# Performance work log

Hardware: AMD Instinct MI355X
Metric: run time of the kernel (lower is better)

The kernel has to match this reference:

```python
import jax, jax.numpy as jnp
import numpy as np

B, L, D, NC, H = 2, 192, 768, 4, 256  # batch, seq_len, bert_hidden, num_case(+coref), hidden


def setup_inputs() -> dict:
    key = jax.random.key(0)
    ks = jax.random.split(key, 9)
    s = 0.02  # init scale
    return {
        "sequence_output": jax.random.normal(ks[0], (B, L, D), dtype=jnp.float32),
        "base_score": jax.random.normal(ks[1], (B, L, NC, L), dtype=jnp.float32),
        "Wp": jax.random.normal(ks[2], (D, H), dtype=jnp.float32) * s,
        "bp": jnp.zeros((H,), dtype=jnp.float32),
        "Wa": jax.random.normal(ks[3], (D, NC * H), dtype=jnp.float32) * s,
        "ba": jnp.zeros((NC * H,), dtype=jnp.float32),
        "Wmid": jax.random.normal(ks[4], (NC, H + NC, H), dtype=jnp.float32) * s,
        "bmid": jnp.zeros((NC, H), dtype=jnp.float32),
        "Wout": jax.random.normal(ks[5], (NC, H), dtype=jnp.float32) * s,
    }


def reference(sequence_output, base_score, Wp, bp, Wa, ba, Wmid, bmid, Wout):
    b, l, d = sequence_output.shape
    nc = Wmid.shape[0]
    h = Wp.shape[1]
    # dropout is identity in eval mode
    h_p = sequence_output @ Wp + bp                       # [B, L, H] (predicate)
    h_a = (sequence_output @ Wa + ba).reshape(b, l, nc, h)  # [B, L, NC, H] (argument)
    # broadcast add: predicate axis p, argument axis a -> [B, P, A, NC, H]
    h_pa = jnp.tanh(h_p[:, :, None, None, :] + h_a[:, None, :, :, :])
    # base_score [B, L, NC, L] -> transpose(2,3) -> [B, P, A, NC], expand over case axis
    bs = jnp.swapaxes(base_score, 2, 3)                   # [B, P, A, NC]
    bs = jnp.broadcast_to(bs[:, :, :, None, :], (b, l, l, nc, nc))
    hcat = jnp.concatenate([h_pa, bs], axis=-1)           # [B, P, A, NC, H+NC]
    # per-case mid Linear, batched as a single einsum over the case axis n
    h_mid = jnp.tanh(jnp.einsum('bpanc,nch->bpanh', hcat, Wmid) + bmid)
    out = jnp.einsum('bpanh,nh->bpan', h_mid, Wout)       # [B, P, A, NC]
    return jnp.transpose(out, (0, 1, 3, 2))               # [B, P, NC, A]
```

## Files before the change

### kernel.cpp

```cpp
#include <hip/hip_runtime.h>

#define LSEQ 192
#define DIM  768
#define NCASE 4
#define HID  256
#define BATCH 2

#define TANH_K 2.885390081777927f

typedef float  floatx4 __attribute__((ext_vector_type(4)));
typedef float  floatx2 __attribute__((ext_vector_type(2)));
typedef __bf16 bf16x8  __attribute__((ext_vector_type(8)));
typedef __bf16 bf16x4  __attribute__((ext_vector_type(4)));

__device__ __forceinline__ float tanh_pre(float x) {
    float e = __builtin_amdgcn_exp2f(x);
    return 1.0f - 2.0f * __builtin_amdgcn_rcpf(e + 1.0f);
}

__device__ __forceinline__ floatx2 pk_fma2(floatx2 a, floatx2 b, floatx2 c) {
    return __builtin_elementwise_fma(a, b, c);
}
__device__ __forceinline__ floatx2 pk_add2(floatx2 a, floatx2 b) { return a + b; }
__device__ __forceinline__ floatx2 pk_mul2(floatx2 a, floatx2 b) { return a * b; }

__device__ __forceinline__ bf16x4 tanh_add4(floatx4 u, floatx4 v) {
    const floatx2 one = {1.0f, 1.0f};
    bf16x4 r;
    #pragma unroll
    for (int i = 0; i < 2; i++) {
        floatx2 tu = {u[2 * i], u[2 * i + 1]};
        floatx2 tv = {v[2 * i], v[2 * i + 1]};
        floatx2 den = pk_fma2(tu, tv, one);
        floatx2 num = pk_add2(tu, tv);
        floatx2 rc;
        rc[0] = __builtin_amdgcn_rcpf(den[0]);
        rc[1] = __builtin_amdgcn_rcpf(den[1]);
        floatx2 res = pk_mul2(num, rc);
        r[2 * i]     = (__bf16)res[0];
        r[2 * i + 1] = (__bf16)res[1];
    }
    return r;
}

__device__ __forceinline__ void barrier_lds_only() {
    __builtin_amdgcn_sched_barrier(0);
    __builtin_amdgcn_s_waitcnt(0xC07F);
    __builtin_amdgcn_s_barrier();
    __builtin_amdgcn_sched_barrier(0);
}

template <int CTRL>
__device__ __forceinline__ float dpp_add(float v) {
    int x = __builtin_amdgcn_update_dpp(0, __builtin_bit_cast(int, v),
                                        CTRL, 0xF, 0xF, true);
    return v + __builtin_bit_cast(float, x);
}
__device__ __forceinline__ float row16_reduce(float v) {
    v = dpp_add<0xB1>(v);
    v = dpp_add<0x4E>(v);
    v = dpp_add<0x141>(v);
    v = dpp_add<0x140>(v);
    return v;
}


__global__ __launch_bounds__(256) void prep(
    const float* __restrict__ seq, const float* __restrict__ Wp,
    const float* __restrict__ Wa,  const float* __restrict__ bp,
    const float* __restrict__ ba,  const float* __restrict__ Wmid,
    const float* __restrict__ bmid,
    float* __restrict__ lin, bf16x8* __restrict__ Bpack)
{
    const int blk = blockIdx.x;
    const int tid = threadIdx.x;

    if (blk >= 1920) {
        int u = (blk - 1920) * 256 + tid;
        int lane = u & 63, f = u >> 6;
        int ct = f & 15, nk = f >> 4;
        int kc = nk % 9, n = nk / 9;
        int h = ct * 16 + (lane & 15);
        int kbase = kc * 32 + ((lane >> 4) & 3) * 8;
        bf16x8 v;
        #pragma unroll
        for (int j = 0; j < 8; j++) {
            int k = kbase + j;
            float x;
            if (k < 260)       x = Wmid[(size_t)(n * 260 + k) * 256 + h];
            else if (k == 260) x = bmid[n * 256 + h];
            else               x = 0.0f;
            v[j] = (__bf16)(TANH_K * x);
        }
        Bpack[u] = v;
        return;
    }

    const int w = tid >> 6, lane = tid & 63;
    const int rt = blk / 80, cg = blk % 80;
    const int quad  = lane >> 4;
    const int col16 = lane & 15;

    __shared__ float cmb[3][256];

    const int arow = rt * 16 + col16;
    const int col  = cg * 16 + col16;
    const int kofs = w * 192;
    const float* aptr = seq + (size_t)arow * DIM + kofs + quad * 8;
    const float* wbase = (cg < 16) ? (Wp + col) : (Wa + (col - 256));
    const int    wstr  = (cg < 16) ? HID : (NCASE * HID);

    floatx4 acc = {};
    floatx4 a0 = *(const floatx4*)(aptr);
    floatx4 a1 = *(const floatx4*)(aptr + 4);
    float bv[8];
    #pragma unroll
    for (int j = 0; j < 8; j++)
        bv[j] = wbase[(size_t)(kofs + quad * 8 + j) * wstr];

    #pragma unroll
    for (int kc = 0; kc < 6; kc++) {
        bf16x8 ah, al, bh, bl;
        #pragma unroll
        for (int j = 0; j < 4; j++) {
            __bf16 h0 = (__bf16)a0[j];
            ah[j] = h0; al[j] = (__bf16)(a0[j] - (float)h0);
            __bf16 h1 = (__bf16)a1[j];
            ah[4 + j] = h1; al[4 + j] = (__bf16)(a1[j] - (float)h1);
        }
        #pragma unroll
        for (int j = 0; j < 8; j++) {
            __bf16 h = (__bf16)bv[j];
            bh[j] = h; bl[j] = (__bf16)(bv[j] - (float)h);
        }
        if (kc < 5) {
            a0 = *(const floatx4*)(aptr + (kc + 1) * 32);
            a1 = *(const floatx4*)(aptr + (kc + 1) * 32 + 4);
            #pragma unroll
            for (int j = 0; j < 8; j++)
                bv[j] = wbase[(size_t)(kofs + (kc + 1) * 32 + quad * 8 + j) * wstr];
        }
        acc = __builtin_amdgcn_mfma_f32_16x16x32_bf16(ah, bh, acc, 0, 0, 0);
        acc = __builtin_amdgcn_mfma_f32_16x16x32_bf16(al, bh, acc, 0, 0, 0);
        acc = __builtin_amdgcn_mfma_f32_16x16x32_bf16(ah, bl, acc, 0, 0, 0);
    }

    if (w > 0) *(floatx4*)&cmb[w - 1][lane * 4] = acc;
    __syncthreads();
    if (w == 0) {
        #pragma unroll
        for (int i = 0; i < 3; i++) {
            floatx4 p = *(const floatx4*)&cmb[i][lane * 4];
            acc += p;
        }
        const float bias = (cg < 16) ? bp[col] : ba[col - 256];
        #pragma unroll
        for (int reg = 0; reg < 4; reg++)
            lin[(size_t)(rt * 16 + quad * 4 + reg) * 1280 + col] =
                tanh_pre(TANH_K * (acc[reg] + bias));
    }
}

__global__ __launch_bounds__(512, 6) void refine_main(
    const float* __restrict__ lin,
    const float* __restrict__ base_score,
    const float* __restrict__ Wout,
    const bf16x8* __restrict__ Bpack,
    float* __restrict__ out)
{
    const int bx = blockIdx.x;
    const int n  = blockIdx.y;
    const int b  = blockIdx.z;
    const int ptile = bx / 24, atile = bx % 24;
    const int p0 = ptile * 8, a0r = atile * 8;

    const int tid   = threadIdx.x;
    const int w     = tid >> 6;
    const int lane  = tid & 63;
    const int quad  = lane >> 4;
    const int col16 = lane & 15;

    __shared__ __align__(16) __bf16 A0[256 * 8];
    __shared__ __align__(16) __bf16 A1[256 * 8];
    __shared__ float red[8][64];

    const int s_g    = tid >> 1;
    const int h2     = tid & 1;
    const int l_g    = s_g & 63;
    const int m_gen  = ((s_g >> 6) << 4) + (l_g & 15);
    const int kq     = (l_g >> 4) * 8 + h2 * 4;
    const int quad_g = l_g >> 4;

    const int pg = p0 + (m_gen >> 3), ag = a0r + (m_gen & 7);
    const float* hp_ptr = lin + (size_t)(b * LSEQ + pg) * 1280 + kq;
    const float* ha_ptr = lin + (size_t)(b * LSEQ + ag) * 1280 + 256 + n * 256 + kq;

    const bf16x8* bbase = Bpack + ((size_t)(n * 9) * 16 + w * 2) * 64 + lane;

    float bs4[4] = {};
    if (quad_g == 0 && h2 == 0) {
        #pragma unroll
        for (int j = 0; j < 4; j++)
            bs4[j] = base_score[((size_t)(b * LSEQ + pg) * NCASE + j) * LSEQ + ag];
    }
    float wo[2];
    #pragma unroll
    for (int ct = 0; ct < 2; ct++)
        wo[ct] = Wout[n * 256 + w * 32 + ct * 16 + col16];

    bf16x8 bcur[2];
    #pragma unroll
    for (int ct = 0; ct < 2; ct++) bcur[ct] = bbase[ct * 64];

    floatx4 hp = *(const floatx4*)(hp_ptr);
    floatx4 ha = *(const floatx4*)(ha_ptr);
    {
        *(bf16x4*)&A0[tid * 4] = tanh_add4(hp, ha);
    }
    hp = *(const floatx4*)(hp_ptr + 32);
    ha = *(const floatx4*)(ha_ptr + 32);
    barrier_lds_only();

    floatx4 acc[4][2] = {};

    #pragma unroll
    for (int kc = 0; kc < 9; kc++) {
        bf16x8 bnext[2];
        if (kc < 8) {
            #pragma unroll
            for (int ct = 0; ct < 2; ct++)
                bnext[ct] = bbase[((kc + 1) * 16 + ct) * 64];
        }
        if (kc < 7) {
            floatx4 u0 = hp, v0 = ha;
            if (kc < 6) {
                hp = *(const floatx4*)(hp_ptr + (kc + 2) * 32);
                ha = *(const floatx4*)(ha_ptr + (kc + 2) * 32);
            }
            __bf16* buf = ((kc + 1) & 1) ? A1 : A0;
            *(bf16x4*)&buf[tid * 4] = tanh_add4(u0, v0);
        } else if (kc == 7) {
            bf16x4 av = {};
            if (quad_g == 0) {
                if (h2 == 0) {
                    #pragma unroll
                    for (int j = 0; j < 4; j++) av[j] = (__bf16)bs4[j];
                } else {
                    av[0] = (__bf16)1.0f;
                }
            }
            *(bf16x4*)&A0[tid * 4] = av;
        }

        const __bf16* rb = (kc & 1) ? A1 : A0;
        bf16x8 af[4];
        #pragma unroll
        for (int rt = 0; rt < 4; rt++)
            af[rt] = *(const bf16x8*)&rb[(rt * 64 + lane) * 8];
        #pragma unroll
        for (int rt = 0; rt < 4; rt++)
            #pragma unroll
            for (int ct = 0; ct < 2; ct++)
                acc[rt][ct] = __builtin_amdgcn_mfma_f32_16x16x32_bf16(
                    af[rt], bcur[ct], acc[rt][ct], 0, 0, 0);
        #pragma unroll
        for (int ct = 0; ct < 2; ct++) bcur[ct] = bnext[ct];
        if (kc < 8) barrier_lds_only();
    }

    const floatx2 onex2 = {1.0f, 1.0f};
    const floatx2 m2x2  = {-2.0f, -2.0f};
    #pragma unroll
    for (int rt = 0; rt < 4; rt++) {
        #pragma unroll
        for (int reg = 0; reg < 4; reg++) {
            floatx2 e;
            e[0] = __builtin_amdgcn_exp2f(acc[rt][0][reg]);
            e[1] = __builtin_amdgcn_exp2f(acc[rt][1][reg]);
            floatx2 d = pk_add2(e, onex2);
            floatx2 rc;
            rc[0] = __builtin_amdgcn_rcpf(d[0]);
            rc[1] = __builtin_amdgcn_rcpf(d[1]);
            floatx2 th = pk_fma2(rc, m2x2, onex2);
            float rs = __builtin_fmaf(th[1], wo[1], th[0] * wo[0]);
            rs = row16_reduce(rs);
            if (col16 == 0) red[w][rt * 16 + quad * 4 + reg] = rs;
        }
    }
    barrier_lds_only();

    if (tid < 64) {
        float total = red[0][tid] + red[1][tid] + red[2][tid] + red[3][tid]
                    + red[4][tid] + red[5][tid] + red[6][tid] + red[7][tid];
        const int p = p0 + (tid >> 3), a = a0r + (tid & 7);
        out[((size_t)(b * LSEQ + p) * NCASE + n) * LSEQ + a] = total;
    }
}

extern "C" void kernel_launch(void* const* d_in, const int* in_sizes, int n_in,
                              void* d_out, int out_size, void* d_ws, size_t ws_size,
                              hipStream_t stream) {
    const float* seq  = (const float*)d_in[0];
    const float* bsc  = (const float*)d_in[1];
    const float* Wp   = (const float*)d_in[2];
    const float* bp   = (const float*)d_in[3];
    const float* Wa   = (const float*)d_in[4];
    const float* ba   = (const float*)d_in[5];
    const float* Wmid = (const float*)d_in[6];
    const float* bmid = (const float*)d_in[7];
    const float* Wout = (const float*)d_in[8];
    float* out = (float*)d_out;

    char* ws = (char*)d_ws;
    float*  lin   = (float*)(ws);
    bf16x8* Bpack = (bf16x8*)(ws + 1966080);

    prep<<<2064, 256, 0, stream>>>(seq, Wp, Wa, bp, ba, Wmid, bmid, lin, Bpack);
    refine_main<<<dim3(576, NCASE, BATCH), 512, 0, stream>>>(
        lin, bsc, Wout, Bpack, out);
}
```

Before: 149.6 us.

## Double the per-block tile and give each wave a 64-row by 64-column MFMA tile

Each block now covers 16 predicates × 8 arguments instead of 8×8, split into two 128-row sub-tiles, and the grid is halved. Each wave computes 4 row tiles × 4 column tiles, so every Bpack (Wmid) fragment loaded from global memory is reused across twice as many rows. Each thread also generates 8 tanh elements per step instead of 4. The aim is to cut redundant weight loads and per-block overhead. In exchange it doubles the accumulator registers, lowers the occupancy hint from 6 to 4, and yields fewer blocks to spread across the CUs.

```diff
diff --git a/kernel.cpp b/kernel.cpp
--- a/kernel.cpp
+++ b/kernel.cpp
@@ -24,13 +24,16 @@
 __device__ __forceinline__ floatx2 pk_add2(floatx2 a, floatx2 b) { return a + b; }
 __device__ __forceinline__ floatx2 pk_mul2(floatx2 a, floatx2 b) { return a * b; }
 
-__device__ __forceinline__ bf16x4 tanh_add4(floatx4 u, floatx4 v) {
+__device__ __forceinline__ bf16x8 tanh_add8(floatx4 u0, floatx4 u1,
+                                            floatx4 v0, floatx4 v1) {
     const floatx2 one = {1.0f, 1.0f};
-    bf16x4 r;
-    #pragma unroll
-    for (int i = 0; i < 2; i++) {
-        floatx2 tu = {u[2 * i], u[2 * i + 1]};
-        floatx2 tv = {v[2 * i], v[2 * i + 1]};
+    float uu[8] = {u0[0], u0[1], u0[2], u0[3], u1[0], u1[1], u1[2], u1[3]};
+    float vv[8] = {v0[0], v0[1], v0[2], v0[3], v1[0], v1[1], v1[2], v1[3]};
+    bf16x8 r;
+    #pragma unroll
+    for (int i = 0; i < 4; i++) {
+        floatx2 tu = {uu[2 * i], uu[2 * i + 1]};
+        floatx2 tv = {vv[2 * i], vv[2 * i + 1]};
         floatx2 den = pk_fma2(tu, tv, one);
         floatx2 num = pk_add2(tu, tv);
         floatx2 rc;
@@ -161,7 +164,7 @@
     }
 }
 
-__global__ __launch_bounds__(512, 6) void refine_main(
+__global__ __launch_bounds__(512, 4) void refine_main(
     const float* __restrict__ lin,
     const float* __restrict__ base_score,
     const float* __restrict__ Wout,
@@ -171,102 +174,103 @@
     const int bx = blockIdx.x;
     const int n  = blockIdx.y;
     const int b  = blockIdx.z;
-    const int ptile = bx / 24, atile = bx % 24;
-    const int p0 = ptile * 8, a0r = atile * 8;
+    const int p0  = (bx / 24) * 16;
+    const int a0r = (bx % 24) * 8;
 
     const int tid   = threadIdx.x;
     const int w     = tid >> 6;
     const int lane  = tid & 63;
     const int quad  = lane >> 4;
     const int col16 = lane & 15;
-
-    __shared__ __align__(16) __bf16 A0[256 * 8];
-    __shared__ __align__(16) __bf16 A1[256 * 8];
+    const int T_r   = w >> 2;
+    const int wq    = w & 3;
+
+    __shared__ __align__(16) __bf16 BUF[2][2][2048];
     __shared__ float red[8][64];
 
-    const int s_g    = tid >> 1;
-    const int h2     = tid & 1;
-    const int l_g    = s_g & 63;
-    const int m_gen  = ((s_g >> 6) << 4) + (l_g & 15);
-    const int kq     = (l_g >> 4) * 8 + h2 * 4;
-    const int quad_g = l_g >> 4;
-
-    const int pg = p0 + (m_gen >> 3), ag = a0r + (m_gen & 7);
-    const float* hp_ptr = lin + (size_t)(b * LSEQ + pg) * 1280 + kq;
-    const float* ha_ptr = lin + (size_t)(b * LSEQ + ag) * 1280 + 256 + n * 256 + kq;
-
-    const bf16x8* bbase = Bpack + ((size_t)(n * 9) * 16 + w * 2) * 64 + lane;
+    const int Tg = tid >> 8;
+    const int u  = tid & 255;
+    const int mg = ((u >> 6) << 4) + (u & 15);
+    const int k0 = ((u >> 4) & 3) * 8;
+    const int pg = p0 + Tg * 8 + (mg >> 3);
+    const int ag = a0r + (mg & 7);
+    const float* hp_ptr = lin + (size_t)(b * LSEQ + pg) * 1280 + k0;
+    const float* ha_ptr = lin + (size_t)(b * LSEQ + ag) * 1280 + 256 + n * 256 + k0;
+    __bf16* wbase = &BUF[Tg][0][u * 8];
+
+    const bf16x8* bb = Bpack + ((size_t)(n * 9) * 16 + wq * 4) * 64 + lane;
 
     float bs4[4] = {};
-    if (quad_g == 0 && h2 == 0) {
+    if (k0 == 0) {
         #pragma unroll
         for (int j = 0; j < 4; j++)
             bs4[j] = base_score[((size_t)(b * LSEQ + pg) * NCASE + j) * LSEQ + ag];
     }
-    float wo[2];
-    #pragma unroll
-    for (int ct = 0; ct < 2; ct++)
-        wo[ct] = Wout[n * 256 + w * 32 + ct * 16 + col16];
-
-    bf16x8 bcur[2];
-    #pragma unroll
-    for (int ct = 0; ct < 2; ct++) bcur[ct] = bbase[ct * 64];
-
-    floatx4 hp = *(const floatx4*)(hp_ptr);
-    floatx4 ha = *(const floatx4*)(ha_ptr);
-    {
-        *(bf16x4*)&A0[tid * 4] = tanh_add4(hp, ha);
-    }
-    hp = *(const floatx4*)(hp_ptr + 32);
-    ha = *(const floatx4*)(ha_ptr + 32);
+
+    bf16x8 bcur[4];
+    #pragma unroll
+    for (int cc = 0; cc < 4; cc++) bcur[cc] = bb[cc * 64];
+
+    floatx4 u0 = *(const floatx4*)(hp_ptr);
+    floatx4 u1 = *(const floatx4*)(hp_ptr + 4);
+    floatx4 v0 = *(const floatx4*)(ha_ptr);
+    floatx4 v1 = *(const floatx4*)(ha_ptr + 4);
+    *(bf16x8*)wbase = tanh_add8(u0, u1, v0, v1);
+    u0 = *(const floatx4*)(hp_ptr + 32);
+    u1 = *(const floatx4*)(hp_ptr + 36);
+    v0 = *(const floatx4*)(ha_ptr + 32);
+    v1 = *(const floatx4*)(ha_ptr + 36);
     barrier_lds_only();
 
-    floatx4 acc[4][2] = {};
+    floatx4 acc[4][4] = {};
 
     #pragma unroll
     for (int kc = 0; kc < 9; kc++) {
-        bf16x8 bnext[2];
+        const __bf16* rb = &BUF[T_r][kc & 1][0];
+        bf16x8 af[4];
+        #pragma unroll
+        for (int rt = 0; rt < 4; rt++)
+            af[rt] = *(const bf16x8*)&rb[(rt * 64 + lane) * 8];
+        #pragma unroll
+        for (int rt = 0; rt < 4; rt++)
+            #pragma unroll
+            for (int cc = 0; cc < 4; cc++)
+                acc[rt][cc] = __builtin_amdgcn_mfma_f32_16x16x32_bf16(
+                    af[rt], bcur[cc], acc[rt][cc], 0, 0, 0);
+
         if (kc < 8) {
             #pragma unroll
-            for (int ct = 0; ct < 2; ct++)
-                bnext[ct] = bbase[((kc + 1) * 16 + ct) * 64];
-        }
+            for (int cc = 0; cc < 4; cc++)
+                bcur[cc] = bb[((kc + 1) * 16 + cc) * 64];
+        }
+
         if (kc < 7) {
-            floatx4 u0 = hp, v0 = ha;
+            floatx4 a0_ = u0, a1_ = u1, b0_ = v0, b1_ = v1;
             if (kc < 6) {
-                hp = *(const floatx4*)(hp_ptr + (kc + 2) * 32);
-                ha = *(const floatx4*)(ha_ptr + (kc + 2) * 32);
+                u0 = *(const floatx4*)(hp_ptr + (kc + 2) * 32);
+                u1 = *(const floatx4*)(hp_ptr + (kc + 2) * 32 + 4);
+                v0 = *(const floatx4*)(ha_ptr + (kc + 2) * 32);
+                v1 = *(const floatx4*)(ha_ptr + (kc + 2) * 32 + 4);
             }
-            __bf16* buf = ((kc + 1) & 1) ? A1 : A0;
-            *(bf16x4*)&buf[tid * 4] = tanh_add4(u0, v0);
+            *(bf16x8*)(wbase + (((kc + 1) & 1) ? 2048 : 0)) =
+                tanh_add8(a0_, a1_, b0_, b1_);
         } else if (kc == 7) {
-            bf16x4 av = {};
-            if (quad_g == 0) {
-                if (h2 == 0) {
-                    #pragma unroll
-                    for (int j = 0; j < 4; j++) av[j] = (__bf16)bs4[j];
-                } else {
-                    av[0] = (__bf16)1.0f;
-                }
+            bf16x8 av = {};
+            if (k0 == 0) {
+                #pragma unroll
+                for (int j = 0; j < 4; j++) av[j] = (__bf16)bs4[j];
+                av[4] = (__bf16)1.0f;
             }
-            *(bf16x4*)&A0[tid * 4] = av;
-        }
-
-        const __bf16* rb = (kc & 1) ? A1 : A0;
-        bf16x8 af[4];
-        #pragma unroll
-        for (int rt = 0; rt < 4; rt++)
-            af[rt] = *(const bf16x8*)&rb[(rt * 64 + lane) * 8];
-        #pragma unroll
-        for (int rt = 0; rt < 4; rt++)
-            #pragma unroll
-            for (int ct = 0; ct < 2; ct++)
-                acc[rt][ct] = __builtin_amdgcn_mfma_f32_16x16x32_bf16(
-                    af[rt], bcur[ct], acc[rt][ct], 0, 0, 0);
-        #pragma unroll
-        for (int ct = 0; ct < 2; ct++) bcur[ct] = bnext[ct];
+            *(bf16x8*)(wbase) = av;
+        }
+
         if (kc < 8) barrier_lds_only();
     }
+
+    float wo[4];
+    #pragma unroll
+    for (int cc = 0; cc < 4; cc++)
+        wo[cc] = Wout[n * 256 + wq * 64 + cc * 16 + col16];
 
     const floatx2 onex2 = {1.0f, 1.0f};
     const floatx2 m2x2  = {-2.0f, -2.0f};
@@ -274,25 +278,35 @@
     for (int rt = 0; rt < 4; rt++) {
         #pragma unroll
         for (int reg = 0; reg < 4; reg++) {
-            floatx2 e;
-            e[0] = __builtin_amdgcn_exp2f(acc[rt][0][reg]);
-            e[1] = __builtin_amdgcn_exp2f(acc[rt][1][reg]);
-            floatx2 d = pk_add2(e, onex2);
-            floatx2 rc;
-            rc[0] = __builtin_amdgcn_rcpf(d[0]);
-            rc[1] = __builtin_amdgcn_rcpf(d[1]);
-            floatx2 th = pk_fma2(rc, m2x2, onex2);
-            float rs = __builtin_fmaf(th[1], wo[1], th[0] * wo[0]);
+            floatx2 e01, e23;
+            e01[0] = __builtin_amdgcn_exp2f(acc[rt][0][reg]);
+            e01[1] = __builtin_amdgcn_exp2f(acc[rt][1][reg]);
+            e23[0] = __builtin_amdgcn_exp2f(acc[rt][2][reg]);
+            e23[1] = __builtin_amdgcn_exp2f(acc[rt][3][reg]);
+            floatx2 d01 = pk_add2(e01, onex2);
+            floatx2 d23 = pk_add2(e23, onex2);
+            floatx2 rc01, rc23;
+            rc01[0] = __builtin_amdgcn_rcpf(d01[0]);
+            rc01[1] = __builtin_amdgcn_rcpf(d01[1]);
+            rc23[0] = __builtin_amdgcn_rcpf(d23[0]);
+            rc23[1] = __builtin_amdgcn_rcpf(d23[1]);
+            floatx2 t01 = pk_fma2(rc01, m2x2, onex2);
+            floatx2 t23 = pk_fma2(rc23, m2x2, onex2);
+            float rs = t01[0] * wo[0];
+            rs = __builtin_fmaf(t01[1], wo[1], rs);
+            rs = __builtin_fmaf(t23[0], wo[2], rs);
+            rs = __builtin_fmaf(t23[1], wo[3], rs);
             rs = row16_reduce(rs);
             if (col16 == 0) red[w][rt * 16 + quad * 4 + reg] = rs;
         }
     }
     barrier_lds_only();
 
-    if (tid < 64) {
-        float total = red[0][tid] + red[1][tid] + red[2][tid] + red[3][tid]
-                    + red[4][tid] + red[5][tid] + red[6][tid] + red[7][tid];
-        const int p = p0 + (tid >> 3), a = a0r + (tid & 7);
+    if (tid < 128) {
+        const int T = tid >> 6, rid = tid & 63;
+        float total = red[T * 4 + 0][rid] + red[T * 4 + 1][rid]
+                    + red[T * 4 + 2][rid] + red[T * 4 + 3][rid];
+        const int p = p0 + T * 8 + (rid >> 3), a = a0r + (rid & 7);
         out[((size_t)(b * LSEQ + p) * NCASE + n) * LSEQ + a] = total;
     }
 }
@@ -316,6 +330,6 @@
     bf16x8* Bpack = (bf16x8*)(ws + 1966080);
 
     prep<<<2064, 256, 0, stream>>>(seq, Wp, Wa, bp, ba, Wmid, bmid, lin, Bpack);
-    refine_main<<<dim3(576, NCASE, BATCH), 512, 0, stream>>>(
+    refine_main<<<dim3(288, NCASE, BATCH), 512, 0, stream>>>(
         lin, bsc, Wout, Bpack, out);
 }
```

Result: slower. 179.7 us (+20.1%).

## Remap MFMA warp tiling to 2 row tiles by 4 column tiles

Applied to the files above, without the earlier changes.

Each of the 8 waves now covers 2 row tiles and 4 column tiles of the 64x256 output, instead of all 4 row tiles and 2 column tiles. This halves the A-fragment LDS reads per wave and doubles the per-wave Bpack global loads. It also shrinks the cross-wave reduction to 4 partials per row and moves the Wout loads after the main loop. Occupancy bounds drop from 6 to 4 blocks to allow more registers for the extra B fragments, which may reduce latency hiding.

```diff
diff --git a/kernel.cpp b/kernel.cpp
--- a/kernel.cpp
+++ b/kernel.cpp
@@ -161,7 +161,7 @@
     }
 }
 
-__global__ __launch_bounds__(512, 6) void refine_main(
+__global__ __launch_bounds__(512, 4) void refine_main(
     const float* __restrict__ lin,
     const float* __restrict__ base_score,
     const float* __restrict__ Wout,
@@ -179,10 +179,12 @@
     const int lane  = tid & 63;
     const int quad  = lane >> 4;
     const int col16 = lane & 15;
+    const int rg    = w >> 2;
+    const int wq    = w & 3;
 
     __shared__ __align__(16) __bf16 A0[256 * 8];
     __shared__ __align__(16) __bf16 A1[256 * 8];
-    __shared__ float red[8][64];
+    __shared__ float red[8][32];
 
     const int s_g    = tid >> 1;
     const int h2     = tid & 1;
@@ -195,7 +197,7 @@
     const float* hp_ptr = lin + (size_t)(b * LSEQ + pg) * 1280 + kq;
     const float* ha_ptr = lin + (size_t)(b * LSEQ + ag) * 1280 + 256 + n * 256 + kq;
 
-    const bf16x8* bbase = Bpack + ((size_t)(n * 9) * 16 + w * 2) * 64 + lane;
+    const bf16x8* bbase = Bpack + ((size_t)(n * 9) * 16 + wq * 4) * 64 + lane;
 
     float bs4[4] = {};
     if (quad_g == 0 && h2 == 0) {
@@ -203,14 +205,10 @@
         for (int j = 0; j < 4; j++)
             bs4[j] = base_score[((size_t)(b * LSEQ + pg) * NCASE + j) * LSEQ + ag];
     }
-    float wo[2];
-    #pragma unroll
-    for (int ct = 0; ct < 2; ct++)
-        wo[ct] = Wout[n * 256 + w * 32 + ct * 16 + col16];
-
-    bf16x8 bcur[2];
-    #pragma unroll
-    for (int ct = 0; ct < 2; ct++) bcur[ct] = bbase[ct * 64];
+
+    bf16x8 bcur[4];
+    #pragma unroll
+    for (int cc = 0; cc < 4; cc++) bcur[cc] = bbase[cc * 64];
 
     floatx4 hp = *(const floatx4*)(hp_ptr);
     floatx4 ha = *(const floatx4*)(ha_ptr);
@@ -221,15 +219,15 @@
     ha = *(const floatx4*)(ha_ptr + 32);
     barrier_lds_only();
 
-    floatx4 acc[4][2] = {};
+    floatx4 acc[2][4] = {};
 
     #pragma unroll
     for (int kc = 0; kc < 9; kc++) {
-        bf16x8 bnext[2];
+        bf16x8 bnext[4];
         if (kc < 8) {
             #pragma unroll
-            for (int ct = 0; ct < 2; ct++)
-                bnext[ct] = bbase[((kc + 1) * 16 + ct) * 64];
+            for (int cc = 0; cc < 4; cc++)
+                bnext[cc] = bbase[((kc + 1) * 16 + cc) * 64];
         }
         if (kc < 7) {
             floatx4 u0 = hp, v0 = ha;
@@ -253,46 +251,62 @@
         }
 
         const __bf16* rb = (kc & 1) ? A1 : A0;
-        bf16x8 af[4];
-        #pragma unroll
-        for (int rt = 0; rt < 4; rt++)
-            af[rt] = *(const bf16x8*)&rb[(rt * 64 + lane) * 8];
-        #pragma unroll
-        for (int rt = 0; rt < 4; rt++)
+        bf16x8 af[2];
+        #pragma unroll
+        for (int rt2 = 0; rt2 < 2; rt2++)
+            af[rt2] = *(const bf16x8*)&rb[((rg * 2 + rt2) * 64 + lane) * 8];
+        #pragma unroll
+        for (int rt2 = 0; rt2 < 2; rt2++)
             #pragma unroll
-            for (int ct = 0; ct < 2; ct++)
-                acc[rt][ct] = __builtin_amdgcn_mfma_f32_16x16x32_bf16(
-                    af[rt], bcur[ct], acc[rt][ct], 0, 0, 0);
-        #pragma unroll
-        for (int ct = 0; ct < 2; ct++) bcur[ct] = bnext[ct];
+            for (int cc = 0; cc < 4; cc++)
+                acc[rt2][cc] = __builtin_amdgcn_mfma_f32_16x16x32_bf16(
+                    af[rt2], bcur[cc], acc[rt2][cc], 0, 0, 0);
+        #pragma unroll
+        for (int cc = 0; cc < 4; cc++) bcur[cc] = bnext[cc];
         if (kc < 8) barrier_lds_only();
     }
+
+    float wo[4];
+    #pragma unroll
+    for (int cc = 0; cc < 4; cc++)
+        wo[cc] = Wout[n * 256 + (wq * 4 + cc) * 16 + col16];
 
     const floatx2 onex2 = {1.0f, 1.0f};
     const floatx2 m2x2  = {-2.0f, -2.0f};
     #pragma unroll
-    for (int rt = 0; rt < 4; rt++) {
+    for (int rt2 = 0; rt2 < 2; rt2++) {
         #pragma unroll
         for (int reg = 0; reg < 4; reg++) {
-            floatx2 e;
-            e[0] = __builtin_amdgcn_exp2f(acc[rt][0][reg]);
-            e[1] = __builtin_amdgcn_exp2f(acc[rt][1][reg]);
-            floatx2 d = pk_add2(e, onex2);
-            floatx2 rc;
-            rc[0] = __builtin_amdgcn_rcpf(d[0]);
-            rc[1] = __builtin_amdgcn_rcpf(d[1]);
-            floatx2 th = pk_fma2(rc, m2x2, onex2);
-            float rs = __builtin_fmaf(th[1], wo[1], th[0] * wo[0]);
+            floatx2 e01, e23;
+            e01[0] = __builtin_amdgcn_exp2f(acc[rt2][0][reg]);
+            e01[1] = __builtin_amdgcn_exp2f(acc[rt2][1][reg]);
+            e23[0] = __builtin_amdgcn_exp2f(acc[rt2][2][reg]);
+            e23[1] = __builtin_amdgcn_exp2f(acc[rt2][3][reg]);
+            floatx2 d01 = pk_add2(e01, onex2);
+            floatx2 d23 = pk_add2(e23, onex2);
+            floatx2 rc01, rc23;
+            rc01[0] = __builtin_amdgcn_rcpf(d01[0]);
+            rc01[1] = __builtin_amdgcn_rcpf(d01[1]);
+            rc23[0] = __builtin_amdgcn_rcpf(d23[0]);
+            rc23[1] = __builtin_amdgcn_rcpf(d23[1]);
+            floatx2 t01 = pk_fma2(rc01, m2x2, onex2);
+            floatx2 t23 = pk_fma2(rc23, m2x2, onex2);
+            float rs = t01[0] * wo[0];
+            rs = __builtin_fmaf(t01[1], wo[1], rs);
+            rs = __builtin_fmaf(t23[0], wo[2], rs);
+            rs = __builtin_fmaf(t23[1], wo[3], rs);
             rs = row16_reduce(rs);
-            if (col16 == 0) red[w][rt * 16 + quad * 4 + reg] = rs;
+            if (col16 == 0) red[w][rt2 * 16 + quad * 4 + reg] = rs;
         }
     }
     barrier_lds_only();
 
     if (tid < 64) {
-        float total = red[0][tid] + red[1][tid] + red[2][tid] + red[3][tid]
-                    + red[4][tid] + red[5][tid] + red[6][tid] + red[7][tid];
-        const int p = p0 + (tid >> 3), a = a0r + (tid & 7);
+        const int m  = tid;
+        const int g  = m >> 5, r5 = m & 31;
+        float total = red[g * 4 + 0][r5] + red[g * 4 + 1][r5]
+                    + red[g * 4 + 2][r5] + red[g * 4 + 3][r5];
+        const int p = p0 + (m >> 3), a = a0r + (m & 7);
         out[((size_t)(b * LSEQ + p) * NCASE + n) * LSEQ + a] = total;
     }
 }
```

Measured after the change: 161.7 us. 1.08x slower.
